# Kernel tuning notes

Measured on AMD Instinct MI355X. Metric: run time of the kernel, lower is better.

## Reference

```python
import jax, jax.numpy as jnp
import numpy as np

D_MODEL = 1024
N_HEADS = 16
D_HEAD = D_MODEL // N_HEADS
LUT_SIZE = 4096
TWO_PI = 2.0 * np.pi
SCALE = np.sqrt(2.0 * D_HEAD).astype(np.float32)

# Global sin/cos lookup table over [0, 2*pi), 4096 entries (mirrors get_global_lut(4096)).
_GRID = (TWO_PI * np.arange(LUT_SIZE) / LUT_SIZE).astype(np.float32)
_SIN_TABLE = jnp.asarray(np.sin(_GRID))
_COS_TABLE = jnp.asarray(np.cos(_GRID))


def _lut_sin_cos(theta):
    # quantize angle to nearest LUT bin (wrap mod 2*pi) and gather
    idx = jnp.mod(jnp.round(theta * (LUT_SIZE / TWO_PI)).astype(jnp.int32), LUT_SIZE)
    return _SIN_TABLE[idx], _COS_TABLE[idx]


def setup_inputs() -> dict:
    key = jax.random.key(0)
    ks = jax.random.split(key, 7)
    B, S = 2, 2048
    x = jax.random.normal(ks[0], (B, S, D_MODEL), dtype=jnp.float32)
    w_q = 0.02 * jax.random.normal(ks[1], (N_HEADS, D_HEAD), dtype=jnp.float32)
    b_q = jnp.zeros((N_HEADS, D_HEAD), dtype=jnp.float32)
    w_k = 0.02 * jax.random.normal(ks[2], (N_HEADS, D_HEAD), dtype=jnp.float32)
    b_k = jnp.zeros((N_HEADS, D_HEAD), dtype=jnp.float32)
    v_w = jax.random.normal(ks[3], (D_MODEL, D_MODEL), dtype=jnp.float32) / np.sqrt(D_MODEL)
    out_w = jax.random.normal(ks[4], (D_MODEL, D_MODEL), dtype=jnp.float32) / np.sqrt(D_MODEL)
    return {"x": x, "w_q": w_q, "b_q": b_q, "w_k": w_k, "b_k": b_k, "v_w": v_w, "out_w": out_w}


def reference(x, w_q, b_q, w_k, b_k, v_w, out_w):
    B, S, D = x.shape
    x_heads = x.reshape(B, S, N_HEADS, D_HEAD)

    theta_q = x_heads / (1.0 + jnp.abs(w_q)) + b_q          # (B,S,H,dh)
    sin_q, cos_q = _lut_sin_cos(theta_q)
    Q = jnp.concatenate([cos_q, sin_q], axis=-1)            # (B,S,H,2dh)

    theta_k = x_heads / (1.0 + jnp.abs(w_k)) + b_k
    sin_k, cos_k = _lut_sin_cos(theta_k)
    K = jnp.concatenate([cos_k, sin_k], axis=-1)            # (B,S,H,2dh)

    V = (x @ v_w.T).reshape(B, S, N_HEADS, D_HEAD)          # (B,S,H,dh)

    scores = jnp.einsum("bqhe,bkhe->bhqk", Q, K) / SCALE    # (B,H,S,S)
    causal = jnp.triu(jnp.ones((S, S), dtype=bool), k=1)
    scores = jnp.where(causal, -jnp.inf, scores)
    attn = jax.nn.softmax(scores, axis=-1)

    out = jnp.einsum("bhqk,bkhd->bqhd", attn, V).reshape(B, S, D)
    return out @ out_w.T
```

## Files before the change

kernel.cpp:

```cpp
#include <hip/hip_runtime.h>
#include <hip/hip_bf16.h>
#include <math.h>


typedef __attribute__((ext_vector_type(8))) __bf16 bf16x8;
typedef __attribute__((ext_vector_type(4))) __bf16 bf16x4;
typedef __attribute__((ext_vector_type(4))) float f32x4;
typedef unsigned short ushort_t;
typedef unsigned int uint_t;

#define LUTC 651.8986469044033f
#define ANG 0.0015339807878856412f
#define QSCL 0.12751743590489435f

__device__ __forceinline__ float fast_exp2(float x) {
#if __has_builtin(__builtin_amdgcn_exp2f)
  return __builtin_amdgcn_exp2f(x);
#else
  return exp2f(x);
#endif
}

__device__ __forceinline__ ushort_t f2bf(float f) {
  union { __bf16 b; ushort_t u; } cv;
  cv.b = (__bf16)f;
  return cv.u;
}

__device__ __forceinline__ void store8(ushort_t* p, const ushort_t v[8]) {
  uint4 u;
  u.x = (uint_t)v[0] | ((uint_t)v[1] << 16);
  u.y = (uint_t)v[2] | ((uint_t)v[3] << 16);
  u.z = (uint_t)v[4] | ((uint_t)v[5] << 16);
  u.w = (uint_t)v[6] | ((uint_t)v[7] << 16);
  *(uint4*)p = u;
}

__device__ __forceinline__ void gl_lds16(const void* g, void* l) {
  __builtin_amdgcn_global_load_lds(
      (__attribute__((address_space(1))) void*)(g),
      (__attribute__((address_space(3))) void*)(l),
      16, 0, 0);
}

__global__ __launch_bounds__(256) void prep_kernel(
    const float* __restrict__ x, const float* __restrict__ wq, const float* __restrict__ bq,
    const float* __restrict__ wk, const float* __restrict__ bk,
    ushort_t* __restrict__ Qs, ushort_t* __restrict__ Ks, ushort_t* __restrict__ xb)
{
  int t = blockIdx.x * 256 + threadIdx.x;
  int dm8 = t & 127;
  int g = t >> 7;
  int dm0 = dm8 * 8;
  int h = dm0 >> 6;

  float aq[8], cq[8], ak[8], ck[8];
#pragma unroll
  for (int j = 0; j < 8; ++j) {
    aq[j] = LUTC / (1.0f + fabsf(wq[dm0 + j]));
    cq[j] = LUTC * bq[dm0 + j];
    ak[j] = LUTC / (1.0f + fabsf(wk[dm0 + j]));
    ck[j] = LUTC * bk[dm0 + j];
  }
  for (int i = 0; i < 4; ++i) {
    int bs = g * 4 + i;
    int b = bs >> 11, s = bs & 2047;
    const float4* xp4 = (const float4*)(x + (size_t)bs * 1024 + dm0);
    float4 xa = xp4[0], xbv4 = xp4[1];
    float xv[8] = {xa.x, xa.y, xa.z, xa.w, xbv4.x, xbv4.y, xbv4.z, xbv4.w};
    ushort_t qc[8], qs[8], kc[8], ks[8], xo[8];
#pragma unroll
    for (int j = 0; j < 8; ++j) {
      int iq = ((int)rintf(fmaf(xv[j], aq[j], cq[j]))) & 4095;
      float sq, cqv;
      __sincosf((float)iq * ANG, &sq, &cqv);
      int ik = ((int)rintf(fmaf(xv[j], ak[j], ck[j]))) & 4095;
      float sk, ckv;
      __sincosf((float)ik * ANG, &sk, &ckv);
      qc[j] = f2bf(cqv * QSCL);
      qs[j] = f2bf(sq * QSCL);
      kc[j] = f2bf(ckv);
      ks[j] = f2bf(sk);
      xo[j] = f2bf(xv[j]);
    }
    size_t qb = ((size_t)(b * 16 + h) * 2048 + s) * 128 + (dm0 & 63);
    store8(Qs + qb, qc);        store8(Qs + qb + 64, qs);
    store8(Ks + qb, kc);        store8(Ks + qb + 64, ks);
    store8(xb + (size_t)bs * 1024 + dm0, xo);
  }
}

__global__ __launch_bounds__(256) void wconv_kernel(
    const float* __restrict__ vw, const float* __restrict__ ow,
    ushort_t* __restrict__ vwb, ushort_t* __restrict__ owb)
{
  int t = blockIdx.x * 256 + threadIdx.x;
  const float* src;
  ushort_t* dst;
  int i;
  if (t < 131072) { src = vw; dst = vwb; i = t; }
  else            { src = ow; dst = owb; i = t - 131072; }
  const float4* p4 = (const float4*)(src + (size_t)i * 8);
  float4 a = p4[0], b = p4[1];
  float v[8] = {a.x, a.y, a.z, a.w, b.x, b.y, b.z, b.w};
  ushort_t o[8];
#pragma unroll
  for (int j = 0; j < 8; ++j) o[j] = f2bf(v[j]);
  store8(dst + (size_t)i * 8, o);
}

template <int EPI>
__global__ __launch_bounds__(256) void gemm_nt(
    const ushort_t* __restrict__ A, const ushort_t* __restrict__ B,
    float* __restrict__ Cf, ushort_t* __restrict__ Cb, int M, int N, int K)
{
  __shared__ __align__(16) ushort_t As[128 * 64];
  __shared__ __align__(16) ushort_t Bs[128 * 64];
  const int l = threadIdx.x & 63;
  const int w = threadIdx.x >> 6;
  const int wm = w >> 1, wn = w & 1;
  const int mt = blockIdx.x % (M >> 7);
  const int nt = blockIdx.x / (M >> 7);
  const int m0 = mt << 7, n0 = nt << 7;

  const f32x4 zero4 = {0.f, 0.f, 0.f, 0.f};
  f32x4 acc[4][4];
#pragma unroll
  for (int i = 0; i < 4; ++i)
#pragma unroll
    for (int j = 0; j < 4; ++j) acc[i][j] = zero4;

  for (int k0 = 0; k0 < K; k0 += 64) {
#pragma unroll
    for (int i = 0; i < 4; ++i) {
      int ci = (w * 4 + i) * 64 + l;
      int r = ci >> 3, c = (ci & 7) ^ (r & 7);
      gl_lds16(A + (size_t)(m0 + r) * K + k0 + c * 8, &As[(w * 4 + i) * 512]);
      gl_lds16(B + (size_t)(n0 + r) * K + k0 + c * 8, &Bs[(w * 4 + i) * 512]);
    }
    __syncthreads();
#pragma unroll
    for (int kk = 0; kk < 2; ++kk) {
      bf16x8 af[4], bfr[4];
#pragma unroll
      for (int mi = 0; mi < 4; ++mi) {
        int r = wm * 64 + mi * 16 + (l & 15);
        int ch = ((l >> 4) + 4 * kk) ^ (r & 7);
        af[mi] = *(const bf16x8*)&As[r * 64 + ch * 8];
      }
#pragma unroll
      for (int ni = 0; ni < 4; ++ni) {
        int r = wn * 64 + ni * 16 + (l & 15);
        int ch = ((l >> 4) + 4 * kk) ^ (r & 7);
        bfr[ni] = *(const bf16x8*)&Bs[r * 64 + ch * 8];
      }
#pragma unroll
      for (int mi = 0; mi < 4; ++mi)
#pragma unroll
        for (int ni = 0; ni < 4; ++ni)
          acc[mi][ni] = __builtin_amdgcn_mfma_f32_16x16x32_bf16(af[mi], bfr[ni], acc[mi][ni], 0, 0, 0);
    }
    __syncthreads();
  }

#pragma unroll
  for (int mi = 0; mi < 4; ++mi)
#pragma unroll
    for (int ni = 0; ni < 4; ++ni)
#pragma unroll
      for (int reg = 0; reg < 4; ++reg) {
        int row = m0 + wm * 64 + mi * 16 + (l >> 4) * 4 + reg;
        int col = n0 + wn * 64 + ni * 16 + (l & 15);
        float v = acc[mi][ni][reg];
        if (EPI == 0) {
          Cf[(size_t)row * N + col] = v;
        } else {
          size_t o = (size_t)(col >> 11) * (1024 * 2048) + (size_t)row * 2048 + (col & 2047);
          Cb[o] = f2bf(v);
        }
      }
}


template<bool MASKED>
__device__ __forceinline__ void attn_tile(
    const ushort_t* __restrict__ Kc, const ushort_t* __restrict__ Vc,
    const bf16x8 (&qf)[2][4], f32x4 (&accO)[2][4], f32x4 (&acc_l)[2],
    int kb, int qw, int lo, int g, const bf16x8& ones)
{
  const f32x4 zero4 = {0.f, 0.f, 0.f, 0.f};
  f32x4 sc[2][4];
#pragma unroll
  for (int qm = 0; qm < 2; ++qm)
#pragma unroll
    for (int ns = 0; ns < 4; ++ns) sc[qm][ns] = zero4;

#pragma unroll
  for (int e = 0; e < 4; ++e) {
#pragma unroll
    for (int ns = 0; ns < 4; ++ns) {
      int kr = ns * 16 + lo;
      int cc = (g + 4 * e) ^ (kr & 7);
      bf16x8 kf = *(const bf16x8*)&Kc[kr * 128 + cc * 8];
#pragma unroll
      for (int qm = 0; qm < 2; ++qm)
        sc[qm][ns] = __builtin_amdgcn_mfma_f32_16x16x32_bf16(kf, qf[qm][e], sc[qm][ns], 0, 0, 0);
    }
  }

  bf16x8 pa[2][2];
#pragma unroll
  for (int qm = 0; qm < 2; ++qm) {
#pragma unroll
    for (int ns = 0; ns < 4; ++ns) {
#pragma unroll
      for (int reg = 0; reg < 4; ++reg) {
        float sv = sc[qm][ns][reg];
        if (MASKED) {
          int ka = kb + ns * 16 + g * 4 + reg;
          int qa = qw + qm * 16 + lo;
          sv = (ka <= qa) ? sv : -__builtin_inff();
        }
        pa[qm][ns >> 1][(ns & 1) * 4 + reg] = (__bf16)fast_exp2(sv);
      }
    }
  }

#pragma unroll
  for (int kk = 0; kk < 2; ++kk) {
#pragma unroll
    for (int nd = 0; nd < 4; ++nd) {
      int vr = nd * 16 + lo;
      int h8 = (g & 1) * 4;
      int cc0 = (4 * kk + (g >> 1)) ^ (vr & 7);
      int cc1 = (4 * kk + 2 + (g >> 1)) ^ (vr & 7);
      union { bf16x8 v8; bf16x4 v4[2]; } u;
      u.v4[0] = *(const bf16x4*)&Vc[vr * 64 + cc0 * 8 + h8];
      u.v4[1] = *(const bf16x4*)&Vc[vr * 64 + cc1 * 8 + h8];
#pragma unroll
      for (int qm = 0; qm < 2; ++qm)
        accO[qm][nd] = __builtin_amdgcn_mfma_f32_16x16x32_bf16(pa[qm][kk], u.v8, accO[qm][nd], 0, 0, 0);
    }
#pragma unroll
    for (int qm = 0; qm < 2; ++qm)
      acc_l[qm] = __builtin_amdgcn_mfma_f32_16x16x32_bf16(pa[qm][kk], ones, acc_l[qm], 0, 0, 0);
  }
}

__global__ __launch_bounds__(256) void attn_kernel(
    const ushort_t* __restrict__ Qs, const ushort_t* __restrict__ Ks,
    const ushort_t* __restrict__ Vt, ushort_t* __restrict__ Ob)
{
  const int S = 2048;
  const int id = blockIdx.x;
  const int bh = id & 31;
  const int qt = (id < 256) ? (15 - (id >> 5)) : ((id - 256) >> 5);
  const int l = threadIdx.x & 63;
  const int w = threadIdx.x >> 6;
  const int g = l >> 4, lo = l & 15;

  __shared__ __align__(16) ushort_t Kl[2][64 * 128];
  __shared__ __align__(16) ushort_t Vl[2][64 * 64];

  const int q0b = qt * 128;
  const int qw = q0b + w * 32;
  const ushort_t* Kbase = Ks + (size_t)bh * S * 128;
  const ushort_t* Vbase = Vt + (size_t)bh * 64 * S;

  bf16x8 ones;
#pragma unroll
  for (int j = 0; j < 8; ++j) ones[j] = (__bf16)1.0f;

  bf16x8 qf[2][4];
#pragma unroll
  for (int qm = 0; qm < 2; ++qm) {
    const ushort_t* qp = Qs + ((size_t)bh * S + qw + qm * 16 + lo) * 128 + 8 * g;
#pragma unroll
    for (int e = 0; e < 4; ++e) qf[qm][e] = *(const bf16x8*)(qp + 32 * e);
  }

  const f32x4 zero4 = {0.f, 0.f, 0.f, 0.f};
  f32x4 accO[2][4];
  f32x4 acc_l[2];
#pragma unroll
  for (int qm = 0; qm < 2; ++qm) {
    acc_l[qm] = zero4;
#pragma unroll
    for (int nd = 0; nd < 4; ++nd) accO[qm][nd] = zero4;
  }

  const int nt = 2 * qt + 2;

#define ATTN_STAGE(buf, kb_)                                                    \
  {                                                                             \
    int kb__ = (kb_);                                                           \
    _Pragma("unroll")                                                           \
    for (int i = 0; i < 4; ++i) {                                               \
      int ci = (w * 4 + i) * 64 + l;                                            \
      int r = ci >> 4, c = (ci & 15) ^ (r & 7);                                 \
      gl_lds16(Kbase + (size_t)(kb__ + r) * 128 + c * 8, &Kl[buf][(w * 4 + i) * 512]); \
    }                                                                           \
    _Pragma("unroll")                                                           \
    for (int i = 0; i < 2; ++i) {                                               \
      int ci = (w * 2 + i) * 64 + l;                                            \
      int r = ci >> 3, c = (ci & 7) ^ (r & 7);                                  \
      gl_lds16(Vbase + (size_t)r * S + kb__ + c * 8, &Vl[buf][(w * 2 + i) * 512]); \
    }                                                                           \
  }

  ATTN_STAGE(0, 0);
  __syncthreads();

  for (int t = 0; t < nt; ++t) {
    int cb = t & 1;
    if (t + 1 < nt) ATTN_STAGE(cb ^ 1, (t + 1) * 64);
    if (t < 2 * qt)
      attn_tile<false>(Kl[cb], Vl[cb], qf, accO, acc_l, t * 64, qw, lo, g, ones);
    else
      attn_tile<true>(Kl[cb], Vl[cb], qf, accO, acc_l, t * 64, qw, lo, g, ones);
    __syncthreads();
  }
#undef ATTN_STAGE

  float linv[2][4];
#pragma unroll
  for (int qm = 0; qm < 2; ++qm)
#pragma unroll
    for (int reg = 0; reg < 4; ++reg)
      linv[qm][reg] = 1.0f / acc_l[qm][reg];

  const int b = bh >> 4, h = bh & 15;
#pragma unroll
  for (int qm = 0; qm < 2; ++qm)
#pragma unroll
    for (int nd = 0; nd < 4; ++nd)
#pragma unroll
      for (int reg = 0; reg < 4; ++reg) {
        int q = qw + qm * 16 + g * 4 + reg;
        int d = nd * 16 + lo;
        Ob[((size_t)(b * 2048 + q)) * 1024 + h * 64 + d] = f2bf(accO[qm][nd][reg] * linv[qm][reg]);
      }
}

extern "C" void kernel_launch(void* const* d_in, const int* in_sizes, int n_in,
                              void* d_out, int out_size, void* d_ws, size_t ws_size,
                              hipStream_t stream) {
  const float* x  = (const float*)d_in[0];
  const float* wq = (const float*)d_in[1];
  const float* bq = (const float*)d_in[2];
  const float* wk = (const float*)d_in[3];
  const float* bk = (const float*)d_in[4];
  const float* vw = (const float*)d_in[5];
  const float* ow = (const float*)d_in[6];
  float* out = (float*)d_out;

  char* ws = (char*)d_ws;
  ushort_t* Qs  = (ushort_t*)(ws);
  ushort_t* Ksb = (ushort_t*)(ws + (16u << 20));
  ushort_t* Vtb = (ushort_t*)(ws + (32u << 20));
  ushort_t* xbb = (ushort_t*)(ws + (40u << 20));
  ushort_t* Obb = (ushort_t*)(ws + (48u << 20));
  ushort_t* vwb = (ushort_t*)(ws + (56u << 20));
  ushort_t* owb = (ushort_t*)(ws + (58u << 20));

  prep_kernel<<<512, 256, 0, stream>>>(x, wq, bq, wk, bk, Qs, Ksb, xbb);
  wconv_kernel<<<1024, 256, 0, stream>>>(vw, ow, vwb, owb);
  gemm_nt<1><<<256, 256, 0, stream>>>(vwb, xbb, nullptr, Vtb, 1024, 4096, 1024);
  attn_kernel<<<512, 256, 0, stream>>>(Qs, Ksb, Vtb, Obb);
  gemm_nt<0><<<256, 256, 0, stream>>>(Obb, owb, out, nullptr, 4096, 1024, 1024);
}
```

Measured before the change: 113.5 us.

## Split heavy causal query tiles across two blocks and merge with combine kernel

```diff
diff --git a/kernel.cpp b/kernel.cpp
--- a/kernel.cpp
+++ b/kernel.cpp
@@ -25,6 +25,12 @@
   union { __bf16 b; ushort_t u; } cv;
   cv.b = (__bf16)f;
   return cv.u;
+}
+
+__device__ __forceinline__ float bf2f(ushort_t u) {
+  union { float f; uint_t u; } cv;
+  cv.u = ((uint_t)u) << 16;
+  return cv.f;
 }
 
 __device__ __forceinline__ void store8(ushort_t* p, const ushort_t v[8]) {
@@ -249,12 +255,20 @@
 
 __global__ __launch_bounds__(256) void attn_kernel(
     const ushort_t* __restrict__ Qs, const ushort_t* __restrict__ Ks,
-    const ushort_t* __restrict__ Vt, ushort_t* __restrict__ Ob)
+    const ushort_t* __restrict__ Vt, ushort_t* __restrict__ Ob,
+    ushort_t* __restrict__ pnB, float* __restrict__ plA, float* __restrict__ plB)
 {
   const int S = 2048;
   const int id = blockIdx.x;
   const int bh = id & 31;
-  const int qt = (id < 256) ? (15 - (id >> 5)) : ((id - 256) >> 5);
+  const int j = (id >> 5) & 7;
+  const int side = id >> 8;
+  const int qtH = 15 - j;
+  const int ntH = 2 * qtH + 2;
+  const int ntL = 2 * j + 2;
+  const int nP1 = ntH - 17;
+  const int seg = bh * 8 + j;
+
   const int l = threadIdx.x & 63;
   const int w = threadIdx.x >> 6;
   const int g = l >> 4, lo = l & 15;
@@ -262,34 +276,14 @@
   __shared__ __align__(16) ushort_t Kl[2][64 * 128];
   __shared__ __align__(16) ushort_t Vl[2][64 * 64];
 
-  const int q0b = qt * 128;
-  const int qw = q0b + w * 32;
   const ushort_t* Kbase = Ks + (size_t)bh * S * 128;
   const ushort_t* Vbase = Vt + (size_t)bh * 64 * S;
+  const int b = bh >> 4, h = bh & 15;
 
   bf16x8 ones;
 #pragma unroll
-  for (int j = 0; j < 8; ++j) ones[j] = (__bf16)1.0f;
-
-  bf16x8 qf[2][4];
-#pragma unroll
-  for (int qm = 0; qm < 2; ++qm) {
-    const ushort_t* qp = Qs + ((size_t)bh * S + qw + qm * 16 + lo) * 128 + 8 * g;
-#pragma unroll
-    for (int e = 0; e < 4; ++e) qf[qm][e] = *(const bf16x8*)(qp + 32 * e);
-  }
-
+  for (int jj = 0; jj < 8; ++jj) ones[jj] = (__bf16)1.0f;
   const f32x4 zero4 = {0.f, 0.f, 0.f, 0.f};
-  f32x4 accO[2][4];
-  f32x4 acc_l[2];
-#pragma unroll
-  for (int qm = 0; qm < 2; ++qm) {
-    acc_l[qm] = zero4;
-#pragma unroll
-    for (int nd = 0; nd < 4; ++nd) accO[qm][nd] = zero4;
-  }
-
-  const int nt = 2 * qt + 2;
 
 #define ATTN_STAGE(buf, kb_)                                                    \
   {                                                                             \
@@ -308,38 +302,157 @@
     }                                                                           \
   }
 
-  ATTN_STAGE(0, 0);
-  __syncthreads();
-
-  for (int t = 0; t < nt; ++t) {
-    int cb = t & 1;
-    if (t + 1 < nt) ATTN_STAGE(cb ^ 1, (t + 1) * 64);
-    if (t < 2 * qt)
-      attn_tile<false>(Kl[cb], Vl[cb], qf, accO, acc_l, t * 64, qw, lo, g, ones);
-    else
-      attn_tile<true>(Kl[cb], Vl[cb], qf, accO, acc_l, t * 64, qw, lo, g, ones);
+  const int qwH = qtH * 128 + w * 32;
+  bf16x8 qfH[2][4];
+#pragma unroll
+  for (int qm = 0; qm < 2; ++qm) {
+    const ushort_t* qp = Qs + ((size_t)bh * S + qwH + qm * 16 + lo) * 128 + 8 * g;
+#pragma unroll
+    for (int e = 0; e < 4; ++e) qfH[qm][e] = *(const bf16x8*)(qp + 32 * e);
+  }
+
+  f32x4 accO[2][4];
+  f32x4 acc_l[2];
+#pragma unroll
+  for (int qm = 0; qm < 2; ++qm) {
+    acc_l[qm] = zero4;
+#pragma unroll
+    for (int nd = 0; nd < 4; ++nd) accO[qm][nd] = zero4;
+  }
+
+  if (side == 0) {
+    ATTN_STAGE(0, 0);
     __syncthreads();
+    for (int s = 0; s < 17; ++s) {
+      int cb = s & 1;
+      if (s + 1 < 17) ATTN_STAGE(cb ^ 1, (s + 1) * 64);
+      if (j == 7 && s == 16)
+        attn_tile<true>(Kl[cb], Vl[cb], qfH, accO, acc_l, s * 64, qwH, lo, g, ones);
+      else
+        attn_tile<false>(Kl[cb], Vl[cb], qfH, accO, acc_l, s * 64, qwH, lo, g, ones);
+      __syncthreads();
+    }
+#pragma unroll
+    for (int qm = 0; qm < 2; ++qm) {
+#pragma unroll
+      for (int nd = 0; nd < 4; ++nd)
+#pragma unroll
+        for (int reg = 0; reg < 4; ++reg) {
+          int q = qwH + qm * 16 + g * 4 + reg;
+          int d = nd * 16 + lo;
+          Ob[((size_t)(b * 2048 + q)) * 1024 + h * 64 + d] = f2bf(accO[qm][nd][reg]);
+        }
+      if (lo == 0) {
+#pragma unroll
+        for (int reg = 0; reg < 4; ++reg)
+          plA[seg * 128 + w * 32 + qm * 16 + g * 4 + reg] = acc_l[qm][reg];
+      }
+    }
+  } else {
+    ATTN_STAGE(0, 17 * 64);
+    __syncthreads();
+    for (int s = 0; s < nP1; ++s) {
+      int cb = s & 1;
+      int sn = s + 1;
+      int kn = (sn < nP1) ? (17 + sn) : (sn - nP1);
+      if (sn < 17) ATTN_STAGE(cb ^ 1, kn * 64);
+      int t = 17 + s;
+      if (s >= 13 - 2 * j)
+        attn_tile<true>(Kl[cb], Vl[cb], qfH, accO, acc_l, t * 64, qwH, lo, g, ones);
+      else
+        attn_tile<false>(Kl[cb], Vl[cb], qfH, accO, acc_l, t * 64, qwH, lo, g, ones);
+      __syncthreads();
+    }
+#pragma unroll
+    for (int qm = 0; qm < 2; ++qm) {
+#pragma unroll
+      for (int nd = 0; nd < 4; ++nd)
+#pragma unroll
+        for (int reg = 0; reg < 4; ++reg) {
+          int qr = w * 32 + qm * 16 + g * 4 + reg;
+          int d = nd * 16 + lo;
+          pnB[((size_t)seg * 128 + qr) * 64 + d] = f2bf(accO[qm][nd][reg]);
+        }
+      if (lo == 0) {
+#pragma unroll
+        for (int reg = 0; reg < 4; ++reg)
+          plB[seg * 128 + w * 32 + qm * 16 + g * 4 + reg] = acc_l[qm][reg];
+      }
+      acc_l[qm] = zero4;
+#pragma unroll
+      for (int nd = 0; nd < 4; ++nd) accO[qm][nd] = zero4;
+    }
+    const int qwL = j * 128 + w * 32;
+    bf16x8 qfL[2][4];
+#pragma unroll
+    for (int qm = 0; qm < 2; ++qm) {
+      const ushort_t* qp = Qs + ((size_t)bh * S + qwL + qm * 16 + lo) * 128 + 8 * g;
+#pragma unroll
+      for (int e = 0; e < 4; ++e) qfL[qm][e] = *(const bf16x8*)(qp + 32 * e);
+    }
+    for (int s2 = 0; s2 < ntL; ++s2) {
+      int s = nP1 + s2;
+      int cb = s & 1;
+      int sn = s + 1;
+      if (sn < 17) ATTN_STAGE(cb ^ 1, (sn - nP1) * 64);
+      if (s2 >= ntL - 2)
+        attn_tile<true>(Kl[cb], Vl[cb], qfL, accO, acc_l, s2 * 64, qwL, lo, g, ones);
+      else
+        attn_tile<false>(Kl[cb], Vl[cb], qfL, accO, acc_l, s2 * 64, qwL, lo, g, ones);
+      __syncthreads();
+    }
+    float linv[2][4];
+#pragma unroll
+    for (int qm = 0; qm < 2; ++qm)
+#pragma unroll
+      for (int reg = 0; reg < 4; ++reg)
+        linv[qm][reg] = 1.0f / acc_l[qm][reg];
+#pragma unroll
+    for (int qm = 0; qm < 2; ++qm)
+#pragma unroll
+      for (int nd = 0; nd < 4; ++nd)
+#pragma unroll
+        for (int reg = 0; reg < 4; ++reg) {
+          int q = qwL + qm * 16 + g * 4 + reg;
+          int d = nd * 16 + lo;
+          Ob[((size_t)(b * 2048 + q)) * 1024 + h * 64 + d] = f2bf(accO[qm][nd][reg] * linv[qm][reg]);
+        }
   }
 #undef ATTN_STAGE
-
-  float linv[2][4];
-#pragma unroll
-  for (int qm = 0; qm < 2; ++qm)
-#pragma unroll
-    for (int reg = 0; reg < 4; ++reg)
-      linv[qm][reg] = 1.0f / acc_l[qm][reg];
-
-  const int b = bh >> 4, h = bh & 15;
-#pragma unroll
-  for (int qm = 0; qm < 2; ++qm)
-#pragma unroll
-    for (int nd = 0; nd < 4; ++nd)
-#pragma unroll
-      for (int reg = 0; reg < 4; ++reg) {
-        int q = qw + qm * 16 + g * 4 + reg;
-        int d = nd * 16 + lo;
-        Ob[((size_t)(b * 2048 + q)) * 1024 + h * 64 + d] = f2bf(accO[qm][nd][reg] * linv[qm][reg]);
-      }
+}
+
+__global__ __launch_bounds__(256) void combine_kernel(
+    ushort_t* __restrict__ Ob, const ushort_t* __restrict__ pnB,
+    const float* __restrict__ plA, const float* __restrict__ plB)
+{
+  int t = blockIdx.x * 256 + threadIdx.x;
+  int d0 = (t & 7) * 8;
+  int qidx = t >> 3;
+  int seg = qidx >> 7, qr = qidx & 127;
+  int bh = seg >> 3, j = seg & 7;
+  int qtH = 15 - j;
+  int b = bh >> 4, h = bh & 15;
+  int qglob = qtH * 128 + qr;
+
+  ushort_t* op = Ob + ((size_t)(b * 2048 + qglob)) * 1024 + h * 64 + d0;
+  const ushort_t* bp = pnB + ((size_t)seg * 128 + qr) * 64 + d0;
+  uint4 ua = *(const uint4*)op;
+  uint4 ub = *(const uint4*)bp;
+  float inv = 1.0f / (plA[seg * 128 + qr] + plB[seg * 128 + qr]);
+
+  const uint_t* pa = (const uint_t*)&ua;
+  const uint_t* pb = (const uint_t*)&ub;
+  ushort_t o[8];
+#pragma unroll
+  for (int i = 0; i < 4; ++i) {
+    float a0 = bf2f((ushort_t)(pa[i] & 0xffff));
+    float a1 = bf2f((ushort_t)(pa[i] >> 16));
+    float b0 = bf2f((ushort_t)(pb[i] & 0xffff));
+    float b1 = bf2f((ushort_t)(pb[i] >> 16));
+    o[2 * i]     = f2bf((a0 + b0) * inv);
+    o[2 * i + 1] = f2bf((a1 + b1) * inv);
+  }
+  store8(op, o);
 }
 
 extern "C" void kernel_launch(void* const* d_in, const int* in_sizes, int n_in,
@@ -363,9 +476,14 @@
   ushort_t* vwb = (ushort_t*)(ws + (56u << 20));
   ushort_t* owb = (ushort_t*)(ws + (58u << 20));
 
+  ushort_t* pnB = (ushort_t*)(ws + (40u << 20));
+  float*    plA = (float*)(ws + (40u << 20) + 4 * 1048576 + 262144);
+  float*    plB = (float*)(ws + (40u << 20) + 4 * 1048576 + 524288);
+
   prep_kernel<<<512, 256, 0, stream>>>(x, wq, bq, wk, bk, Qs, Ksb, xbb);
   wconv_kernel<<<1024, 256, 0, stream>>>(vw, ow, vwb, owb);
   gemm_nt<1><<<256, 256, 0, stream>>>(vwb, xbb, nullptr, Vtb, 1024, 4096, 1024);
-  attn_kernel<<<512, 256, 0, stream>>>(Qs, Ksb, Vtb, Obb);
+  attn_kernel<<<512, 256, 0, stream>>>(Qs, Ksb, Vtb, Obb, pnB, plA, plB);
+  combine_kernel<<<1024, 256, 0, stream>>>(Obb, pnB, plA, plB);
   gemm_nt<0><<<256, 256, 0, stream>>>(Obb, owb, out, nullptr, 4096, 1024, 1024);
 }
```

Measured after the change: 130.5 us. 15.0% more time.

## Store Q/K/V in MFMA fragment layout and run LDS-free single-wave attention

Applied to the files above, without the earlier changes.

```diff
diff --git a/kernel.cpp b/kernel.cpp
--- a/kernel.cpp
+++ b/kernel.cpp
@@ -4,7 +4,6 @@
 
 
 typedef __attribute__((ext_vector_type(8))) __bf16 bf16x8;
-typedef __attribute__((ext_vector_type(4))) __bf16 bf16x4;
 typedef __attribute__((ext_vector_type(4))) float f32x4;
 typedef unsigned short ushort_t;
 typedef unsigned int uint_t;
@@ -46,47 +45,58 @@
 __global__ __launch_bounds__(256) void prep_kernel(
     const float* __restrict__ x, const float* __restrict__ wq, const float* __restrict__ bq,
     const float* __restrict__ wk, const float* __restrict__ bk,
-    ushort_t* __restrict__ Qs, ushort_t* __restrict__ Ks, ushort_t* __restrict__ xb)
-{
-  int t = blockIdx.x * 256 + threadIdx.x;
-  int dm8 = t & 127;
-  int g = t >> 7;
-  int dm0 = dm8 * 8;
-  int h = dm0 >> 6;
-
-  float aq[8], cq[8], ak[8], ck[8];
-#pragma unroll
-  for (int j = 0; j < 8; ++j) {
-    aq[j] = LUTC / (1.0f + fabsf(wq[dm0 + j]));
-    cq[j] = LUTC * bq[dm0 + j];
-    ak[j] = LUTC / (1.0f + fabsf(wk[dm0 + j]));
-    ck[j] = LUTC * bk[dm0 + j];
-  }
-  for (int i = 0; i < 4; ++i) {
-    int bs = g * 4 + i;
-    int b = bs >> 11, s = bs & 2047;
-    const float4* xp4 = (const float4*)(x + (size_t)bs * 1024 + dm0);
-    float4 xa = xp4[0], xbv4 = xp4[1];
-    float xv[8] = {xa.x, xa.y, xa.z, xa.w, xbv4.x, xbv4.y, xbv4.z, xbv4.w};
+    ushort_t* __restrict__ Qf, ushort_t* __restrict__ Kf, ushort_t* __restrict__ xb)
+{
+  const int lo = threadIdx.x & 15;
+  const int dq = threadIdx.x >> 4;
+  const int blk = blockIdx.x;
+  const int sb = blk >> 1;
+  const int half = blk & 1;
+  const int tok = sb * 16 + lo;
+  const int b = tok >> 11;
+  const int s16 = sb & 127;
+
+#pragma unroll
+  for (int r = 0; r < 4; ++r) {
+    const int dm0 = dq * 8 + (half * 4 + r) * 128;
+    const int h = dm0 >> 6;
+    const int dc = dm0 & 63;
+    const int e = dc >> 5, gp = (dc >> 3) & 3;
+    const int bh = b * 16 + h;
+
+    float aq[8], cq[8], ak[8], ck[8];
+#pragma unroll
+    for (int jj = 0; jj < 8; ++jj) {
+      aq[jj] = LUTC / (1.0f + fabsf(wq[dm0 + jj]));
+      cq[jj] = LUTC * bq[dm0 + jj];
+      ak[jj] = LUTC / (1.0f + fabsf(wk[dm0 + jj]));
+      ck[jj] = LUTC * bk[dm0 + jj];
+    }
+    const float4* xp4 = (const float4*)(x + (size_t)tok * 1024 + dm0);
+    float4 xa = xp4[0], xbv = xp4[1];
+    float xv[8] = {xa.x, xa.y, xa.z, xa.w, xbv.x, xbv.y, xbv.z, xbv.w};
     ushort_t qc[8], qs[8], kc[8], ks[8], xo[8];
 #pragma unroll
-    for (int j = 0; j < 8; ++j) {
-      int iq = ((int)rintf(fmaf(xv[j], aq[j], cq[j]))) & 4095;
+    for (int jj = 0; jj < 8; ++jj) {
+      int iq = ((int)rintf(fmaf(xv[jj], aq[jj], cq[jj]))) & 4095;
       float sq, cqv;
       __sincosf((float)iq * ANG, &sq, &cqv);
-      int ik = ((int)rintf(fmaf(xv[j], ak[j], ck[j]))) & 4095;
+      int ik = ((int)rintf(fmaf(xv[jj], ak[jj], ck[jj]))) & 4095;
       float sk, ckv;
       __sincosf((float)ik * ANG, &sk, &ckv);
-      qc[j] = f2bf(cqv * QSCL);
-      qs[j] = f2bf(sq * QSCL);
-      kc[j] = f2bf(ckv);
-      ks[j] = f2bf(sk);
-      xo[j] = f2bf(xv[j]);
-    }
-    size_t qb = ((size_t)(b * 16 + h) * 2048 + s) * 128 + (dm0 & 63);
-    store8(Qs + qb, qc);        store8(Qs + qb + 64, qs);
-    store8(Ks + qb, kc);        store8(Ks + qb + 64, ks);
-    store8(xb + (size_t)bs * 1024 + dm0, xo);
+      qc[jj] = f2bf(cqv * QSCL);
+      qs[jj] = f2bf(sq * QSCL);
+      kc[jj] = f2bf(ckv);
+      ks[jj] = f2bf(sk);
+      xo[jj] = f2bf(xv[jj]);
+    }
+    size_t fb = ((size_t)bh * 128 + s16) * 4;
+    size_t ln = (size_t)(gp * 16 + lo) * 8;
+    store8(Qf + (fb + e) * 512 + ln, qc);
+    store8(Qf + (fb + 2 + e) * 512 + ln, qs);
+    store8(Kf + (fb + e) * 512 + ln, kc);
+    store8(Kf + (fb + 2 + e) * 512 + ln, ks);
+    store8(xb + (size_t)tok * 1024 + dm0, xo);
   }
 }
 
@@ -175,7 +185,11 @@
         if (EPI == 0) {
           Cf[(size_t)row * N + col] = v;
         } else {
-          size_t o = (size_t)(col >> 11) * (1024 * 2048) + (size_t)row * 2048 + (col & 2047);
+          int hh = row >> 6, dh = row & 63, nd = dh >> 4, lov = dh & 15;
+          int bb = col >> 11, ss = col & 2047, kt = ss >> 6, sk = ss & 63;
+          int kk2 = sk >> 5, gg = (sk >> 2) & 3, jj = ((sk >> 4) & 1) * 4 + (sk & 3);
+          size_t o = ((((size_t)(bb * 16 + hh) * 32 + kt) * 8 + kk2 * 4 + nd) * 64
+                      + gg * 16 + lov) * 8 + jj;
           Cb[o] = f2bf(v);
         }
       }
@@ -183,162 +197,119 @@
 
 
 template<bool MASKED>
-__device__ __forceinline__ void attn_tile(
-    const ushort_t* __restrict__ Kc, const ushort_t* __restrict__ Vc,
-    const bf16x8 (&qf)[2][4], f32x4 (&accO)[2][4], f32x4 (&acc_l)[2],
-    int kb, int qw, int lo, int g, const bf16x8& ones)
-{
+__device__ __forceinline__ void attn_step64(
+    const ushort_t* __restrict__ kp, const ushort_t* __restrict__ vp,
+    const bf16x8 (&qf)[4][4], f32x4 (&accO)[4][4], float (&lsum)[4],
+    int g, int lo)
+{
+  bf16x8 vf[8];
+#pragma unroll
+  for (int i = 0; i < 8; ++i) vf[i] = *(const bf16x8*)(vp + i * 512);
+
   const f32x4 zero4 = {0.f, 0.f, 0.f, 0.f};
-  f32x4 sc[2][4];
-#pragma unroll
-  for (int qm = 0; qm < 2; ++qm)
-#pragma unroll
-    for (int ns = 0; ns < 4; ++ns) sc[qm][ns] = zero4;
-
-#pragma unroll
-  for (int e = 0; e < 4; ++e) {
-#pragma unroll
-    for (int ns = 0; ns < 4; ++ns) {
-      int kr = ns * 16 + lo;
-      int cc = (g + 4 * e) ^ (kr & 7);
-      bf16x8 kf = *(const bf16x8*)&Kc[kr * 128 + cc * 8];
-#pragma unroll
-      for (int qm = 0; qm < 2; ++qm)
-        sc[qm][ns] = __builtin_amdgcn_mfma_f32_16x16x32_bf16(kf, qf[qm][e], sc[qm][ns], 0, 0, 0);
-    }
-  }
-
-  bf16x8 pa[2][2];
-#pragma unroll
-  for (int qm = 0; qm < 2; ++qm) {
-#pragma unroll
-    for (int ns = 0; ns < 4; ++ns) {
+  bf16x8 pa[4][2];
+#pragma unroll
+  for (int ns = 0; ns < 4; ++ns) {
+    f32x4 sc[4];
+#pragma unroll
+    for (int qm = 0; qm < 4; ++qm) sc[qm] = zero4;
+#pragma unroll
+    for (int e = 0; e < 4; ++e) {
+      bf16x8 kf = *(const bf16x8*)(kp + (ns * 4 + e) * 512);
+#pragma unroll
+      for (int qm = 0; qm < 4; ++qm)
+        sc[qm] = __builtin_amdgcn_mfma_f32_16x16x32_bf16(kf, qf[qm][e], sc[qm], 0, 0, 0);
+    }
+#pragma unroll
+    for (int qm = 0; qm < 4; ++qm)
 #pragma unroll
       for (int reg = 0; reg < 4; ++reg) {
-        float sv = sc[qm][ns][reg];
-        if (MASKED) {
-          int ka = kb + ns * 16 + g * 4 + reg;
-          int qa = qw + qm * 16 + lo;
-          sv = (ka <= qa) ? sv : -__builtin_inff();
-        }
-        pa[qm][ns >> 1][(ns & 1) * 4 + reg] = (__bf16)fast_exp2(sv);
-      }
-    }
-  }
-
-#pragma unroll
-  for (int kk = 0; kk < 2; ++kk) {
+        float sv = sc[qm][reg];
+        if (MASKED)
+          sv = ((ns * 16 + g * 4 + reg) <= (qm * 16 + lo)) ? sv : -__builtin_inff();
+        float pv = fast_exp2(sv);
+        lsum[qm] += pv;
+        pa[qm][ns >> 1][(ns & 1) * 4 + reg] = (__bf16)pv;
+      }
+  }
+#pragma unroll
+  for (int kk = 0; kk < 2; ++kk)
 #pragma unroll
     for (int nd = 0; nd < 4; ++nd) {
-      int vr = nd * 16 + lo;
-      int h8 = (g & 1) * 4;
-      int cc0 = (4 * kk + (g >> 1)) ^ (vr & 7);
-      int cc1 = (4 * kk + 2 + (g >> 1)) ^ (vr & 7);
-      union { bf16x8 v8; bf16x4 v4[2]; } u;
-      u.v4[0] = *(const bf16x4*)&Vc[vr * 64 + cc0 * 8 + h8];
-      u.v4[1] = *(const bf16x4*)&Vc[vr * 64 + cc1 * 8 + h8];
-#pragma unroll
-      for (int qm = 0; qm < 2; ++qm)
-        accO[qm][nd] = __builtin_amdgcn_mfma_f32_16x16x32_bf16(pa[qm][kk], u.v8, accO[qm][nd], 0, 0, 0);
-    }
-#pragma unroll
-    for (int qm = 0; qm < 2; ++qm)
-      acc_l[qm] = __builtin_amdgcn_mfma_f32_16x16x32_bf16(pa[qm][kk], ones, acc_l[qm], 0, 0, 0);
-  }
-}
-
-__global__ __launch_bounds__(256) void attn_kernel(
-    const ushort_t* __restrict__ Qs, const ushort_t* __restrict__ Ks,
-    const ushort_t* __restrict__ Vt, ushort_t* __restrict__ Ob)
-{
-  const int S = 2048;
+      bf16x8 vv = vf[kk * 4 + nd];
+#pragma unroll
+      for (int qm = 0; qm < 4; ++qm)
+        accO[qm][nd] = __builtin_amdgcn_mfma_f32_16x16x32_bf16(pa[qm][kk], vv, accO[qm][nd], 0, 0, 0);
+    }
+}
+
+__global__ __launch_bounds__(64) void attn_kernel(
+    const ushort_t* __restrict__ Qf, const ushort_t* __restrict__ Kf,
+    const ushort_t* __restrict__ Vf, ushort_t* __restrict__ Ob)
+{
   const int id = blockIdx.x;
   const int bh = id & 31;
-  const int qt = (id < 256) ? (15 - (id >> 5)) : ((id - 256) >> 5);
-  const int l = threadIdx.x & 63;
-  const int w = threadIdx.x >> 6;
+  const int j = (id >> 5) & 7;
+  const int s = id >> 8;
+  const int p = s >> 1;
+  const int m = (j + p) & 7;
+  const int qt = (s & 1) ? m : 15 - m;
+  const int h2 = p;
+  const int qbase = qt * 128 + h2 * 64;
+  const int ntk = 2 * qt + h2 + 1;
+
+  const int l = threadIdx.x;
   const int g = l >> 4, lo = l & 15;
 
-  __shared__ __align__(16) ushort_t Kl[2][64 * 128];
-  __shared__ __align__(16) ushort_t Vl[2][64 * 64];
-
-  const int q0b = qt * 128;
-  const int qw = q0b + w * 32;
-  const ushort_t* Kbase = Ks + (size_t)bh * S * 128;
-  const ushort_t* Vbase = Vt + (size_t)bh * 64 * S;
-
-  bf16x8 ones;
-#pragma unroll
-  for (int j = 0; j < 8; ++j) ones[j] = (__bf16)1.0f;
-
-  bf16x8 qf[2][4];
-#pragma unroll
-  for (int qm = 0; qm < 2; ++qm) {
-    const ushort_t* qp = Qs + ((size_t)bh * S + qw + qm * 16 + lo) * 128 + 8 * g;
-#pragma unroll
-    for (int e = 0; e < 4; ++e) qf[qm][e] = *(const bf16x8*)(qp + 32 * e);
+  bf16x8 qf[4][4];
+  {
+    const ushort_t* qp = Qf + ((size_t)bh * 128 + (qbase >> 4)) * 4 * 512 + (size_t)l * 8;
+#pragma unroll
+    for (int qm = 0; qm < 4; ++qm)
+#pragma unroll
+      for (int e = 0; e < 4; ++e)
+        qf[qm][e] = *(const bf16x8*)(qp + (qm * 4 + e) * 512);
   }
 
   const f32x4 zero4 = {0.f, 0.f, 0.f, 0.f};
-  f32x4 accO[2][4];
-  f32x4 acc_l[2];
-#pragma unroll
-  for (int qm = 0; qm < 2; ++qm) {
-    acc_l[qm] = zero4;
+  f32x4 accO[4][4];
+  float lsum[4] = {0.f, 0.f, 0.f, 0.f};
+#pragma unroll
+  for (int qm = 0; qm < 4; ++qm)
 #pragma unroll
     for (int nd = 0; nd < 4; ++nd) accO[qm][nd] = zero4;
-  }
-
-  const int nt = 2 * qt + 2;
-
-#define ATTN_STAGE(buf, kb_)                                                    \
-  {                                                                             \
-    int kb__ = (kb_);                                                           \
-    _Pragma("unroll")                                                           \
-    for (int i = 0; i < 4; ++i) {                                               \
-      int ci = (w * 4 + i) * 64 + l;                                            \
-      int r = ci >> 4, c = (ci & 15) ^ (r & 7);                                 \
-      gl_lds16(Kbase + (size_t)(kb__ + r) * 128 + c * 8, &Kl[buf][(w * 4 + i) * 512]); \
-    }                                                                           \
-    _Pragma("unroll")                                                           \
-    for (int i = 0; i < 2; ++i) {                                               \
-      int ci = (w * 2 + i) * 64 + l;                                            \
-      int r = ci >> 3, c = (ci & 7) ^ (r & 7);                                  \
-      gl_lds16(Vbase + (size_t)r * S + kb__ + c * 8, &Vl[buf][(w * 2 + i) * 512]); \
-    }                                                                           \
-  }
-
-  ATTN_STAGE(0, 0);
-  __syncthreads();
-
-  for (int t = 0; t < nt; ++t) {
-    int cb = t & 1;
-    if (t + 1 < nt) ATTN_STAGE(cb ^ 1, (t + 1) * 64);
-    if (t < 2 * qt)
-      attn_tile<false>(Kl[cb], Vl[cb], qf, accO, acc_l, t * 64, qw, lo, g, ones);
-    else
-      attn_tile<true>(Kl[cb], Vl[cb], qf, accO, acc_l, t * 64, qw, lo, g, ones);
-    __syncthreads();
-  }
-#undef ATTN_STAGE
-
-  float linv[2][4];
-#pragma unroll
-  for (int qm = 0; qm < 2; ++qm)
+
+  const ushort_t* kp = Kf + (size_t)bh * 262144 + (size_t)l * 8;
+  const ushort_t* vp = Vf + (size_t)bh * 131072 + (size_t)l * 8;
+
+  int t = 0;
+  for (; t < ntk - 1; ++t)
+    attn_step64<false>(kp + (size_t)t * 8192, vp + (size_t)t * 4096, qf, accO, lsum, g, lo);
+  attn_step64<true>(kp + (size_t)t * 8192, vp + (size_t)t * 4096, qf, accO, lsum, g, lo);
+
+#pragma unroll
+  for (int qm = 0; qm < 4; ++qm) {
+    lsum[qm] += __shfl_xor(lsum[qm], 16);
+    lsum[qm] += __shfl_xor(lsum[qm], 32);
+  }
+  float linv[4][4];
+#pragma unroll
+  for (int qm = 0; qm < 4; ++qm)
 #pragma unroll
     for (int reg = 0; reg < 4; ++reg)
-      linv[qm][reg] = 1.0f / acc_l[qm][reg];
-
-  const int b = bh >> 4, h = bh & 15;
-#pragma unroll
-  for (int qm = 0; qm < 2; ++qm)
+      linv[qm][reg] = 1.0f / __shfl(lsum[qm], g * 4 + reg);
+
+  const int b = bh >> 4, hh = bh & 15;
+#pragma unroll
+  for (int qm = 0; qm < 4; ++qm)
 #pragma unroll
     for (int nd = 0; nd < 4; ++nd)
 #pragma unroll
       for (int reg = 0; reg < 4; ++reg) {
-        int q = qw + qm * 16 + g * 4 + reg;
+        int q = qbase + qm * 16 + g * 4 + reg;
         int d = nd * 16 + lo;
-        Ob[((size_t)(b * 2048 + q)) * 1024 + h * 64 + d] = f2bf(accO[qm][nd][reg] * linv[qm][reg]);
+        Ob[((size_t)(b * 2048 + q)) * 1024 + hh * 64 + d] =
+            f2bf(accO[qm][nd][reg] * linv[qm][reg]);
       }
 }
 
@@ -355,17 +326,17 @@
   float* out = (float*)d_out;
 
   char* ws = (char*)d_ws;
-  ushort_t* Qs  = (ushort_t*)(ws);
-  ushort_t* Ksb = (ushort_t*)(ws + (16u << 20));
-  ushort_t* Vtb = (ushort_t*)(ws + (32u << 20));
+  ushort_t* Qfb = (ushort_t*)(ws);
+  ushort_t* Kfb = (ushort_t*)(ws + (16u << 20));
+  ushort_t* Vfb = (ushort_t*)(ws + (32u << 20));
   ushort_t* xbb = (ushort_t*)(ws + (40u << 20));
   ushort_t* Obb = (ushort_t*)(ws + (48u << 20));
   ushort_t* vwb = (ushort_t*)(ws + (56u << 20));
   ushort_t* owb = (ushort_t*)(ws + (58u << 20));
 
-  prep_kernel<<<512, 256, 0, stream>>>(x, wq, bq, wk, bk, Qs, Ksb, xbb);
+  prep_kernel<<<512, 256, 0, stream>>>(x, wq, bq, wk, bk, Qfb, Kfb, xbb);
   wconv_kernel<<<1024, 256, 0, stream>>>(vw, ow, vwb, owb);
-  gemm_nt<1><<<256, 256, 0, stream>>>(vwb, xbb, nullptr, Vtb, 1024, 4096, 1024);
-  attn_kernel<<<512, 256, 0, stream>>>(Qs, Ksb, Vtb, Obb);
+  gemm_nt<1><<<256, 256, 0, stream>>>(vwb, xbb, nullptr, Vfb, 1024, 4096, 1024);
+  attn_kernel<<<1024, 64, 0, stream>>>(Qfb, Kfb, Vfb, Obb);
   gemm_nt<0><<<256, 256, 0, stream>>>(Obb, owb, out, nullptr, 4096, 1024, 1024);
 }
```

New measurement: 150.4 us. +32.5%, slower.
